# Kernel tuning notes

Hardware: AMD Instinct MI355X
Metric: run time of the kernel (lower is better)

Reference implementation:

```python
import jax, jax.numpy as jnp
import numpy as np

B, S, D, H = 2, 2048, 1024, 16
HD = D // H


def alibi_slopes(num_heads):
    x = (2.0 ** 8) ** (1.0 / num_heads)
    return jnp.array([1.0 / x ** (i + 1) for i in range(num_heads)], dtype=jnp.float32)


def setup_inputs() -> dict:
    key = jax.random.key(0)
    ks = jax.random.split(key, 5)
    scale = 1.0 / np.sqrt(D)
    return {
        "x": jax.random.normal(ks[0], (B, S, D), dtype=jnp.float32),
        "Wq": jax.random.normal(ks[1], (D, D), dtype=jnp.float32) * scale,
        "Wk": jax.random.normal(ks[2], (D, D), dtype=jnp.float32) * scale,
        "Wv": jax.random.normal(ks[3], (D, D), dtype=jnp.float32) * scale,
        "Wo": jax.random.normal(ks[4], (D, D), dtype=jnp.float32) * scale,
    }


def reference(x, Wq, Wk, Wv, Wo):
    b, s, d = x.shape
    # nn.Linear(bias=False): y = x @ W.T
    q = (x @ Wq.T).reshape(b, s, H, HD).transpose(0, 2, 1, 3)  # [b,h,s,hd]
    k = (x @ Wk.T).reshape(b, s, H, HD).transpose(0, 2, 1, 3)
    v = (x @ Wv.T).reshape(b, s, H, HD).transpose(0, 2, 1, 3)

    scores = jnp.einsum("bhqd,bhkd->bhqk", q, k) / jnp.sqrt(jnp.float32(HD))
    rel = (jnp.arange(s)[None, :] - jnp.arange(s)[:, None]).astype(jnp.float32)  # x - y
    m = alibi_slopes(H)[:, None, None]  # [h,1,1]
    scores = scores - (m * rel)[None]  # subtract bias, as in source

    causal_mask = jnp.tril(jnp.ones((s, s), dtype=bool))
    scores = jnp.where(causal_mask[None, None], scores, -jnp.inf)

    attn = jax.nn.softmax(scores, axis=-1)
    out = jnp.einsum("bhqk,bhkd->bhqd", attn, v)
    out = out.transpose(0, 2, 1, 3).reshape(b, s, d)
    return out @ Wo.T
```

## Files before the change

kernel.cpp:

```cpp
#include <hip/hip_runtime.h>

typedef __attribute__((ext_vector_type(8))) short bf16x8;
typedef __attribute__((ext_vector_type(4))) float f32x4;
typedef __attribute__((ext_vector_type(16))) float f32x16;
typedef __attribute__((ext_vector_type(8))) unsigned short u16x8;
typedef __attribute__((ext_vector_type(4))) unsigned short u16x4;
typedef __attribute__((ext_vector_type(2))) unsigned int uint2v;

#define MFMA_16x16x32(a, b, c) __builtin_amdgcn_mfma_f32_16x16x32_bf16((a), (b), (c), 0, 0, 0)
#define MFMA32(a, b, c) __builtin_amdgcn_mfma_f32_32x32x16_bf16((a), (b), (c), 0, 0, 0)

__device__ __forceinline__ unsigned short f2bf(float f) {
  unsigned u = __builtin_bit_cast(unsigned, f);
  u += 0x7fffu + ((u >> 16) & 1u);
  return (unsigned short)(u >> 16);
}

__device__ __forceinline__ void gload_lds16(const void* g, void* l) {
  __builtin_amdgcn_global_load_lds((__attribute__((address_space(1))) void*)(g),
                                   (__attribute__((address_space(3))) void*)(l),
                                   16, 0, 0);
}

__device__ __forceinline__ unsigned cvtpk(float lo, float hi) {
  unsigned r;
  asm("v_cvt_pk_bf16_f32 %0, %1, %2" : "=v"(r) : "v"(lo), "v"(hi));
  return r;
}

__global__ void cvt_bf16(const float* __restrict__ src, unsigned short* __restrict__ dst, int n4) {
  int i = blockIdx.x * blockDim.x + threadIdx.x;
  if (i >= n4) return;
  f32x4 v = *(const f32x4*)(src + (size_t)i * 4);
  u16x4 o;
  o.x = f2bf(v.x); o.y = f2bf(v.y); o.z = f2bf(v.z); o.w = f2bf(v.w);
  *(u16x4*)(dst + (size_t)i * 4) = o;
}

__global__ void cvt_w4(const float* __restrict__ s0, const float* __restrict__ s1,
                       const float* __restrict__ s2, const float* __restrict__ s3,
                       unsigned short* __restrict__ d0, unsigned short* __restrict__ d1,
                       unsigned short* __restrict__ d2, unsigned short* __restrict__ d3,
                       int n4) {
  const float* s; unsigned short* d;
  switch (blockIdx.y) {
    case 0: s = s0; d = d0; break;
    case 1: s = s1; d = d1; break;
    case 2: s = s2; d = d2; break;
    default: s = s3; d = d3; break;
  }
  int i = blockIdx.x * blockDim.x + threadIdx.x;
  if (i >= n4) return;
  f32x4 v = *(const f32x4*)(s + (size_t)i * 4);
  u16x4 o;
  o.x = f2bf(v.x); o.y = f2bf(v.y); o.z = f2bf(v.z); o.w = f2bf(v.w);
  *(u16x4*)(d + (size_t)i * 4) = o;
}

template <int OUTMODE>
__device__ __forceinline__ void gemm_body(const unsigned short* __restrict__ A,
                                          const unsigned short* __restrict__ Bw,
                                          void* __restrict__ Cout, float scale,
                                          int bx, int by) {
  constexpr int K = 1024, N = 1024;
  __shared__ unsigned short As[128 * 32];
  __shared__ unsigned short Bs[128 * 32];
  const int tid = threadIdx.x;
  const int lane = tid & 63;
  const int wave = tid >> 6;
  const int wm = (wave >> 1) * 64;
  const int wn = (wave & 1) * 64;
  const int l15 = lane & 15, lg = lane >> 4;

  f32x4 acc[4][4];
#pragma unroll
  for (int mi = 0; mi < 4; ++mi)
#pragma unroll
    for (int ni = 0; ni < 4; ++ni) acc[mi][ni] = (f32x4){0.f, 0.f, 0.f, 0.f};

  const int r0 = tid >> 2;
  const int c0 = (tid & 3) * 8;
  const unsigned short* Ag = A + (size_t)(by * 128 + r0) * K + c0;
  const unsigned short* Bg = Bw + (size_t)(bx * 128 + r0) * K + c0;
  unsigned short* lA = As + tid * 8;
  unsigned short* lB = Bs + tid * 8;

  for (int kt = 0; kt < K / 32; ++kt) {
    __syncthreads();
    gload_lds16(Ag + kt * 32, lA);
    gload_lds16(Ag + (size_t)64 * K + kt * 32, lA + 2048);
    gload_lds16(Bg + kt * 32, lB);
    gload_lds16(Bg + (size_t)64 * K + kt * 32, lB + 2048);
    __syncthreads();

    bf16x8 af[4], bf[4];
#pragma unroll
    for (int mi = 0; mi < 4; ++mi)
      af[mi] = *(const bf16x8*)&As[(wm + mi * 16 + l15) * 32 + lg * 8];
#pragma unroll
    for (int ni = 0; ni < 4; ++ni)
      bf[ni] = *(const bf16x8*)&Bs[(wn + ni * 16 + l15) * 32 + lg * 8];
#pragma unroll
    for (int mi = 0; mi < 4; ++mi)
#pragma unroll
      for (int ni = 0; ni < 4; ++ni)
        acc[mi][ni] = MFMA_16x16x32(af[mi], bf[ni], acc[mi][ni]);
  }

#pragma unroll
  for (int mi = 0; mi < 4; ++mi) {
    const int row = by * 128 + wm + mi * 16 + lg * 4;
#pragma unroll
    for (int ni = 0; ni < 4; ++ni) {
      const int col = bx * 128 + wn + ni * 16 + l15;
#pragma unroll
      for (int i = 0; i < 4; ++i) {
        float v = acc[mi][ni][i];
        if constexpr (OUTMODE == 0) {
          ((unsigned short*)Cout)[(size_t)(row + i) * N + col] = f2bf(v * scale);
        } else if constexpr (OUTMODE == 1) {
          const int m = row + i, n = col;
          ((unsigned short*)Cout)[(size_t)(((m >> 11) * 16 + (n >> 6)) * 64 + (n & 63)) * 2048 +
                                  (m & 2047)] = f2bf(v);
        } else {
          ((float*)Cout)[(size_t)(row + i) * N + col] = v;
        }
      }
    }
  }
}

__global__ __launch_bounds__(256) void gemm_qkv(const unsigned short* __restrict__ A,
                                                const unsigned short* __restrict__ Wq,
                                                const unsigned short* __restrict__ Wk,
                                                const unsigned short* __restrict__ Wv,
                                                unsigned short* __restrict__ Qo,
                                                unsigned short* __restrict__ Ko,
                                                unsigned short* __restrict__ Vo) {
  const int z = blockIdx.z;
  if (z == 0)      gemm_body<0>(A, Wq, Qo, 0.18033688011112042f, blockIdx.x, blockIdx.y);
  else if (z == 1) gemm_body<0>(A, Wk, Ko, 1.0f, blockIdx.x, blockIdx.y);
  else             gemm_body<1>(A, Wv, Vo, 1.0f, blockIdx.x, blockIdx.y);
}

__global__ __launch_bounds__(256) void gemm_out(const unsigned short* __restrict__ A,
                                                const unsigned short* __restrict__ Bw,
                                                float* __restrict__ C) {
  gemm_body<2>(A, Bw, C, 1.0f, blockIdx.x, blockIdx.y);
}

__global__ __launch_bounds__(256, 2) void attn_fwd(const unsigned short* __restrict__ Qg,
                                                   const unsigned short* __restrict__ Kg,
                                                   const unsigned short* __restrict__ Vtg,
                                                   unsigned short* __restrict__ Og) {
  constexpr int S = 2048;
  const int bid = blockIdx.x;
  const int xcd = bid & 7;
  const int ii = bid >> 3;
  const int hi2 = ii >> 5;
  const int jj = ii & 31;
  const int x = hi2 ? (15 - (jj & 15)) : (jj & 15);
  const int bh = xcd * 4 + hi2 * 2 + (jj >> 4);
  const int b = bh >> 4, h = bh & 15;

  const int lane = threadIdx.x & 63;
  const int wave = threadIdx.x >> 6;
  const int ql = lane & 31;
  const int H = lane >> 5;
  const int qw0 = x * 128 + wave * 32;
  const int qg = qw0 + ql;
  const float slope = exp2f(-0.5f * (float)(h + 1));
  const float sl2 = slope * 1.44269504088896f;

  bf16x8 qf[4];
  {
    const unsigned short* qp = Qg + (size_t)(b * S + qg) * 1024 + h * 64 + H * 8;
#pragma unroll
    for (int c = 0; c < 4; ++c) qf[c] = *(const bf16x8*)(qp + 16 * c);
  }

  f32x16 nbj;
#pragma unroll
  for (int r = 0; r < 16; ++r) {
    const float crow = (float)((r & 3) + 8 * (r >> 2) + 4 * H);
    nbj[r] = -sl2 * crow;
  }

  const unsigned short* kp0 = Kg + (size_t)(b * S + ql) * 1024 + h * 64 + H * 8;
  const unsigned short* kp1 = kp0 + (size_t)32 * 1024;
  const unsigned short* vp0 = Vtg + (size_t)(bh * 64 + ql) * S + H * 8;
  const unsigned short* vp1 = vp0 + (size_t)32 * S;

  f32x16 o0, o1;
#pragma unroll
  for (int r = 0; r < 16; ++r) { o0[r] = 0.f; o1[r] = 0.f; }
  float m = -1e30f, l = 0.f;

  const int nt = ((qw0 + 31) >> 6) + 1;
  for (int t = 0; t < nt; ++t) {
    const int k0 = t * 64;
    bf16x8 kf0[4], kf1[4], vf0[4], vf1[4];
#pragma unroll
    for (int c = 0; c < 4; ++c) {
      kf0[c] = *(const bf16x8*)(kp0 + 16 * c);
      kf1[c] = *(const bf16x8*)(kp1 + 16 * c);
      vf0[c] = *(const bf16x8*)(vp0 + 16 * c);
      vf1[c] = *(const bf16x8*)(vp1 + 16 * c);
    }
    kp0 += 65536; kp1 += 65536; vp0 += 64; vp1 += 64;

    f32x16 s0 = MFMA32(kf0[0], qf[0], nbj);
    f32x16 s1 = MFMA32(kf1[0], qf[0], nbj);
#pragma unroll
    for (int c = 1; c < 4; ++c) {
      s0 = MFMA32(kf0[c], qf[c], s0);
      s1 = MFMA32(kf1[c], qf[c], s1);
    }

    if (t == nt - 1) {
      const int qk = qg - k0 - 4 * H;
#pragma unroll
      for (int r = 0; r < 16; ++r) {
        const int crow = (r & 3) + 8 * (r >> 2);
        s0[r] = (crow > qk) ? -1e30f : s0[r];
        s1[r] = (crow + 32 > qk) ? -1e30f : s1[r];
      }
    }

    const float vb0 = sl2 * (float)k0;
    const float vb1 = sl2 * (float)(k0 + 32);
    float mx0 = s0[0], mx1 = s1[0];
#pragma unroll
    for (int r = 1; r < 16; ++r) { mx0 = fmaxf(mx0, s0[r]); mx1 = fmaxf(mx1, s1[r]); }
    float tmax = fmaxf(mx0 - vb0, mx1 - vb1);
    tmax = fmaxf(tmax, __shfl_xor(tmax, 32, 64));
    const float mnew = fmaxf(m, tmax);
    const float corr = __builtin_amdgcn_exp2f(m - mnew);
    m = mnew;
    const float e0 = vb0 + mnew, e1 = vb1 + mnew;

    f32x16 pp0, pp1;
#pragma unroll
    for (int r = 0; r < 16; ++r) {
      pp0[r] = __builtin_amdgcn_exp2f(s0[r] - e0);
      pp1[r] = __builtin_amdgcn_exp2f(s1[r] - e1);
    }
    float t8[8];
#pragma unroll
    for (int r = 0; r < 8; ++r) t8[r] = (pp0[r] + pp0[r + 8]) + (pp1[r] + pp1[r + 8]);
    float tsum = ((t8[0] + t8[1]) + (t8[2] + t8[3])) + ((t8[4] + t8[5]) + (t8[6] + t8[7]));
    tsum += __shfl_xor(tsum, 32, 64);
    l = l * corr + tsum;

#pragma unroll
    for (int r = 0; r < 16; ++r) { o0[r] *= corr; o1[r] *= corr; }

#pragma unroll
    for (int ck = 0; ck < 4; ++ck) {
      const int c = ck & 1;
      unsigned w0, w1, w2, w3;
      if (ck < 2) {
        w0 = cvtpk(pp0[8 * c + 0], pp0[8 * c + 1]);
        w1 = cvtpk(pp0[8 * c + 2], pp0[8 * c + 3]);
        w2 = cvtpk(pp0[8 * c + 4], pp0[8 * c + 5]);
        w3 = cvtpk(pp0[8 * c + 6], pp0[8 * c + 7]);
      } else {
        w0 = cvtpk(pp1[8 * c + 0], pp1[8 * c + 1]);
        w1 = cvtpk(pp1[8 * c + 2], pp1[8 * c + 3]);
        w2 = cvtpk(pp1[8 * c + 4], pp1[8 * c + 5]);
        w3 = cvtpk(pp1[8 * c + 6], pp1[8 * c + 7]);
      }
      unsigned sa = H ? w0 : w2;
      unsigned sb = H ? w1 : w3;
      sa = (unsigned)__shfl_xor((int)sa, 32, 64);
      sb = (unsigned)__shfl_xor((int)sb, 32, 64);
      union { unsigned u[4]; bf16x8 v; } fr;
      fr.u[0] = H ? sa : w0;
      fr.u[1] = H ? sb : w1;
      fr.u[2] = H ? w2 : sa;
      fr.u[3] = H ? w3 : sb;
      o0 = MFMA32(vf0[ck], fr.v, o0);
      o1 = MFMA32(vf1[ck], fr.v, o1);
    }
  }

  const float rl = __builtin_amdgcn_rcpf(l);
  unsigned short* ob = Og + (size_t)(b * S + qg) * 1024 + h * 64 + 4 * H;
#pragma unroll
  for (int a2 = 0; a2 < 4; ++a2) {
    uint2v w01, w23;
    w01.x = cvtpk(o0[4 * a2 + 0] * rl, o0[4 * a2 + 1] * rl);
    w01.y = cvtpk(o0[4 * a2 + 2] * rl, o0[4 * a2 + 3] * rl);
    w23.x = cvtpk(o1[4 * a2 + 0] * rl, o1[4 * a2 + 1] * rl);
    w23.y = cvtpk(o1[4 * a2 + 2] * rl, o1[4 * a2 + 3] * rl);
    *(uint2v*)(ob + 8 * a2) = w01;
    *(uint2v*)(ob + 32 + 8 * a2) = w23;
  }
}

extern "C" void kernel_launch(void* const* d_in, const int* in_sizes, int n_in,
                              void* d_out, int out_size, void* d_ws, size_t ws_size,
                              hipStream_t stream) {
  const float* x = (const float*)d_in[0];
  const float* Wq = (const float*)d_in[1];
  const float* Wk = (const float*)d_in[2];
  const float* Wv = (const float*)d_in[3];
  const float* Wo = (const float*)d_in[4];

  unsigned short* xb = (unsigned short*)d_ws;
  unsigned short* Wqb = xb + 4194304;
  unsigned short* Wkb = Wqb + 1048576;
  unsigned short* Wvb = Wkb + 1048576;
  unsigned short* Wob = Wvb + 1048576;
  unsigned short* Qb = Wob + 1048576;
  unsigned short* Kb = Qb + 4194304;
  unsigned short* Vtb = Kb + 4194304;
  unsigned short* Ob = Vtb + 4194304;

  cvt_bf16<<<4096, 256, 0, stream>>>(x, xb, 1048576);
  cvt_w4<<<dim3(1024, 4), 256, 0, stream>>>(Wq, Wk, Wv, Wo, Wqb, Wkb, Wvb, Wob, 262144);

  gemm_qkv<<<dim3(8, 32, 3), 256, 0, stream>>>(xb, Wqb, Wkb, Wvb, Qb, Kb, Vtb);

  attn_fwd<<<512, 256, 0, stream>>>(Qb, Kb, Vtb, Ob);

  gemm_out<<<dim3(8, 32), 256, 0, stream>>>(Ob, Wob, (float*)d_out);
}
```

Before: 212.0 us.

## Split attention KV range across waves with LDS combine and double-buffered loads

Each block now handles one 32-row query tile, and its four waves split the causal KV range into chunks, each running its own online softmax. The per-wave max, sum and output partials are merged through shared memory, with serialized accumulation across the waves. K/V fragment loads are double-buffered across tiles, and s_setprio is raised around the MFMAs. The goal is more parallelism (2048 blocks instead of 512) and better latency hiding. The cost is more redundant Q loads, LDS traffic and barriers, and higher register pressure.

```diff
diff --git a/kernel.cpp b/kernel.cpp
--- a/kernel.cpp
+++ b/kernel.cpp
@@ -149,26 +149,116 @@
   gemm_body<2>(A, Bw, C, 1.0f, blockIdx.x, blockIdx.y);
 }
 
+
+#define LOADT(KA, KB, VA, VB, tt)                                          \
+  {                                                                        \
+    const unsigned short* _kp = kbase + (size_t)(tt) * 65536;              \
+    const unsigned short* _vp = vbase + (size_t)(tt) * 64;                 \
+    _Pragma("unroll")                                                      \
+    for (int c = 0; c < 4; ++c) {                                          \
+      KA[c] = *(const bf16x8*)(_kp + 16 * c);                              \
+      KB[c] = *(const bf16x8*)(_kp + 32768 + 16 * c);                      \
+      VA[c] = *(const bf16x8*)(_vp + 16 * c);                              \
+      VB[c] = *(const bf16x8*)(_vp + 65536 + 16 * c);                      \
+    }                                                                      \
+  }
+
+#define COMPT(KA, KB, VA, VB, tt, MASKED)                                      \
+  {                                                                            \
+    const int _k0 = (tt) * 64;                                                 \
+    __builtin_amdgcn_s_setprio(1);                                             \
+    f32x16 _s0 = MFMA32(KA[0], qf[0], nbj);                                    \
+    f32x16 _s1 = MFMA32(KB[0], qf[0], nbj);                                    \
+    _s0 = MFMA32(KA[1], qf[1], _s0); _s1 = MFMA32(KB[1], qf[1], _s1);          \
+    _s0 = MFMA32(KA[2], qf[2], _s0); _s1 = MFMA32(KB[2], qf[2], _s1);          \
+    _s0 = MFMA32(KA[3], qf[3], _s0); _s1 = MFMA32(KB[3], qf[3], _s1);          \
+    __builtin_amdgcn_s_setprio(0);                                             \
+    if (MASKED) {                                                              \
+      const int _qk = qg - _k0 - 4 * H;                                        \
+      _Pragma("unroll")                                                        \
+      for (int r = 0; r < 16; ++r) {                                           \
+        const int _cr = (r & 3) + 8 * (r >> 2);                                \
+        _s0[r] = (_cr > _qk) ? -1e30f : _s0[r];                                \
+        _s1[r] = (_cr + 32 > _qk) ? -1e30f : _s1[r];                           \
+      }                                                                        \
+    }                                                                          \
+    const float _vb0 = sl2 * (float)_k0;                                       \
+    const float _vb1 = sl2 * (float)(_k0 + 32);                                \
+    float _mx0 = _s0[0], _mx1 = _s1[0];                                        \
+    _Pragma("unroll")                                                          \
+    for (int r = 1; r < 16; ++r) { _mx0 = fmaxf(_mx0, _s0[r]); _mx1 = fmaxf(_mx1, _s1[r]); } \
+    float _tmax = fmaxf(_mx0 - _vb0, _mx1 - _vb1);                             \
+    _tmax = fmaxf(_tmax, __shfl_xor(_tmax, 32, 64));                           \
+    const float _mnew = fmaxf(m, _tmax);                                       \
+    const float _corr = __builtin_amdgcn_exp2f(m - _mnew);                     \
+    m = _mnew;                                                                 \
+    const float _e0 = _vb0 + _mnew, _e1 = _vb1 + _mnew;                        \
+    f32x16 _pp0, _pp1;                                                         \
+    _Pragma("unroll")                                                          \
+    for (int r = 0; r < 16; ++r) {                                             \
+      _pp0[r] = __builtin_amdgcn_exp2f(_s0[r] - _e0);                          \
+      _pp1[r] = __builtin_amdgcn_exp2f(_s1[r] - _e1);                          \
+    }                                                                          \
+    float _t8[8];                                                              \
+    _Pragma("unroll")                                                          \
+    for (int r = 0; r < 8; ++r) _t8[r] = (_pp0[r] + _pp0[r + 8]) + (_pp1[r] + _pp1[r + 8]); \
+    float _tsum = ((_t8[0] + _t8[1]) + (_t8[2] + _t8[3])) + ((_t8[4] + _t8[5]) + (_t8[6] + _t8[7])); \
+    _tsum += __shfl_xor(_tsum, 32, 64);                                        \
+    l = l * _corr + _tsum;                                                     \
+    _Pragma("unroll")                                                          \
+    for (int r = 0; r < 16; ++r) { o0[r] *= _corr; o1[r] *= _corr; }           \
+    _Pragma("unroll")                                                          \
+    for (int ck = 0; ck < 4; ++ck) {                                           \
+      const int _c = ck & 1;                                                   \
+      unsigned _w0, _w1, _w2, _w3;                                             \
+      if (ck < 2) {                                                            \
+        _w0 = cvtpk(_pp0[8 * _c + 0], _pp0[8 * _c + 1]);                       \
+        _w1 = cvtpk(_pp0[8 * _c + 2], _pp0[8 * _c + 3]);                       \
+        _w2 = cvtpk(_pp0[8 * _c + 4], _pp0[8 * _c + 5]);                       \
+        _w3 = cvtpk(_pp0[8 * _c + 6], _pp0[8 * _c + 7]);                       \
+      } else {                                                                 \
+        _w0 = cvtpk(_pp1[8 * _c + 0], _pp1[8 * _c + 1]);                       \
+        _w1 = cvtpk(_pp1[8 * _c + 2], _pp1[8 * _c + 3]);                       \
+        _w2 = cvtpk(_pp1[8 * _c + 4], _pp1[8 * _c + 5]);                       \
+        _w3 = cvtpk(_pp1[8 * _c + 6], _pp1[8 * _c + 7]);                       \
+      }                                                                        \
+      unsigned _sa = H ? _w0 : _w2;                                            \
+      unsigned _sb = H ? _w1 : _w3;                                            \
+      _sa = (unsigned)__shfl_xor((int)_sa, 32, 64);                            \
+      _sb = (unsigned)__shfl_xor((int)_sb, 32, 64);                            \
+      union { unsigned u[4]; bf16x8 v; } _fr;                                  \
+      _fr.u[0] = H ? _sa : _w0;                                                \
+      _fr.u[1] = H ? _sb : _w1;                                                \
+      _fr.u[2] = H ? _w2 : _sa;                                                \
+      _fr.u[3] = H ? _w3 : _sb;                                                \
+      __builtin_amdgcn_s_setprio(1);                                           \
+      o0 = MFMA32(VA[ck], _fr.v, o0);                                          \
+      o1 = MFMA32(VB[ck], _fr.v, o1);                                          \
+      __builtin_amdgcn_s_setprio(0);                                           \
+    }                                                                          \
+  }
+
 __global__ __launch_bounds__(256, 2) void attn_fwd(const unsigned short* __restrict__ Qg,
                                                    const unsigned short* __restrict__ Kg,
                                                    const unsigned short* __restrict__ Vtg,
                                                    unsigned short* __restrict__ Og) {
   constexpr int S = 2048;
+  __shared__ float Ml[4][64];
+  __shared__ float Ll[4][64];
+  __shared__ float Oacc[64][33];
+
   const int bid = blockIdx.x;
   const int xcd = bid & 7;
-  const int ii = bid >> 3;
-  const int hi2 = ii >> 5;
-  const int jj = ii & 31;
-  const int x = hi2 ? (15 - (jj & 15)) : (jj & 15);
-  const int bh = xcd * 4 + hi2 * 2 + (jj >> 4);
+  const int ord = bid >> 3;
+  const int qt = 63 - (ord >> 2);
+  const int bh = xcd * 4 + (ord & 3);
   const int b = bh >> 4, h = bh & 15;
 
   const int lane = threadIdx.x & 63;
   const int wave = threadIdx.x >> 6;
   const int ql = lane & 31;
   const int H = lane >> 5;
-  const int qw0 = x * 128 + wave * 32;
-  const int qg = qw0 + ql;
+  const int qg = qt * 32 + ql;
   const float slope = exp2f(-0.5f * (float)(h + 1));
   const float sl2 = slope * 1.44269504088896f;
 
@@ -186,115 +276,84 @@
     nbj[r] = -sl2 * crow;
   }
 
-  const unsigned short* kp0 = Kg + (size_t)(b * S + ql) * 1024 + h * 64 + H * 8;
-  const unsigned short* kp1 = kp0 + (size_t)32 * 1024;
-  const unsigned short* vp0 = Vtg + (size_t)(bh * 64 + ql) * S + H * 8;
-  const unsigned short* vp1 = vp0 + (size_t)32 * S;
+  const unsigned short* kbase = Kg + (size_t)(b * S + ql) * 1024 + h * 64 + H * 8;
+  const unsigned short* vbase = Vtg + (size_t)(bh * 64 + ql) * S + H * 8;
 
   f32x16 o0, o1;
 #pragma unroll
   for (int r = 0; r < 16; ++r) { o0[r] = 0.f; o1[r] = 0.f; }
   float m = -1e30f, l = 0.f;
 
-  const int nt = ((qw0 + 31) >> 6) + 1;
-  for (int t = 0; t < nt; ++t) {
-    const int k0 = t * 64;
-    bf16x8 kf0[4], kf1[4], vf0[4], vf1[4];
-#pragma unroll
-    for (int c = 0; c < 4; ++c) {
-      kf0[c] = *(const bf16x8*)(kp0 + 16 * c);
-      kf1[c] = *(const bf16x8*)(kp1 + 16 * c);
-      vf0[c] = *(const bf16x8*)(vp0 + 16 * c);
-      vf1[c] = *(const bf16x8*)(vp1 + 16 * c);
-    }
-    kp0 += 65536; kp1 += 65536; vp0 += 64; vp1 += 64;
-
-    f32x16 s0 = MFMA32(kf0[0], qf[0], nbj);
-    f32x16 s1 = MFMA32(kf1[0], qf[0], nbj);
-#pragma unroll
-    for (int c = 1; c < 4; ++c) {
-      s0 = MFMA32(kf0[c], qf[c], s0);
-      s1 = MFMA32(kf1[c], qf[c], s1);
-    }
-
-    if (t == nt - 1) {
-      const int qk = qg - k0 - 4 * H;
-#pragma unroll
-      for (int r = 0; r < 16; ++r) {
-        const int crow = (r & 3) + 8 * (r >> 2);
-        s0[r] = (crow > qk) ? -1e30f : s0[r];
-        s1[r] = (crow + 32 > qk) ? -1e30f : s1[r];
+  const int nt = (qt >> 1) + 1;
+  const int cs = (nt + 3) >> 2;
+  const int t0 = wave * cs;
+  const int te = min(nt, t0 + cs);
+
+  bf16x8 ka0[4], ka1[4], vA0[4], vA1[4];
+  bf16x8 kb0[4], kb1[4], vB0[4], vB1[4];
+
+  if (t0 < te) {
+    LOADT(ka0, ka1, vA0, vA1, t0);
+    int t = t0;
+    for (; t + 1 < te; ++t) {
+      if ((t - t0) & 1) {
+        LOADT(ka0, ka1, vA0, vA1, t + 1);
+        COMPT(kb0, kb1, vB0, vB1, t, false);
+      } else {
+        LOADT(kb0, kb1, vB0, vB1, t + 1);
+        COMPT(ka0, ka1, vA0, vA1, t, false);
       }
     }
-
-    const float vb0 = sl2 * (float)k0;
-    const float vb1 = sl2 * (float)(k0 + 32);
-    float mx0 = s0[0], mx1 = s1[0];
-#pragma unroll
-    for (int r = 1; r < 16; ++r) { mx0 = fmaxf(mx0, s0[r]); mx1 = fmaxf(mx1, s1[r]); }
-    float tmax = fmaxf(mx0 - vb0, mx1 - vb1);
-    tmax = fmaxf(tmax, __shfl_xor(tmax, 32, 64));
-    const float mnew = fmaxf(m, tmax);
-    const float corr = __builtin_amdgcn_exp2f(m - mnew);
-    m = mnew;
-    const float e0 = vb0 + mnew, e1 = vb1 + mnew;
-
-    f32x16 pp0, pp1;
-#pragma unroll
-    for (int r = 0; r < 16; ++r) {
-      pp0[r] = __builtin_amdgcn_exp2f(s0[r] - e0);
-      pp1[r] = __builtin_amdgcn_exp2f(s1[r] - e1);
+    const bool msk = (te == nt);
+    if ((t - t0) & 1) {
+      COMPT(kb0, kb1, vB0, vB1, t, msk);
+    } else {
+      COMPT(ka0, ka1, vA0, vA1, t, msk);
     }
-    float t8[8];
-#pragma unroll
-    for (int r = 0; r < 8; ++r) t8[r] = (pp0[r] + pp0[r + 8]) + (pp1[r] + pp1[r + 8]);
-    float tsum = ((t8[0] + t8[1]) + (t8[2] + t8[3])) + ((t8[4] + t8[5]) + (t8[6] + t8[7]));
-    tsum += __shfl_xor(tsum, 32, 64);
-    l = l * corr + tsum;
-
-#pragma unroll
-    for (int r = 0; r < 16; ++r) { o0[r] *= corr; o1[r] *= corr; }
-
-#pragma unroll
-    for (int ck = 0; ck < 4; ++ck) {
-      const int c = ck & 1;
-      unsigned w0, w1, w2, w3;
-      if (ck < 2) {
-        w0 = cvtpk(pp0[8 * c + 0], pp0[8 * c + 1]);
-        w1 = cvtpk(pp0[8 * c + 2], pp0[8 * c + 3]);
-        w2 = cvtpk(pp0[8 * c + 4], pp0[8 * c + 5]);
-        w3 = cvtpk(pp0[8 * c + 6], pp0[8 * c + 7]);
-      } else {
-        w0 = cvtpk(pp1[8 * c + 0], pp1[8 * c + 1]);
-        w1 = cvtpk(pp1[8 * c + 2], pp1[8 * c + 3]);
-        w2 = cvtpk(pp1[8 * c + 4], pp1[8 * c + 5]);
-        w3 = cvtpk(pp1[8 * c + 6], pp1[8 * c + 7]);
-      }
-      unsigned sa = H ? w0 : w2;
-      unsigned sb = H ? w1 : w3;
-      sa = (unsigned)__shfl_xor((int)sa, 32, 64);
-      sb = (unsigned)__shfl_xor((int)sb, 32, 64);
-      union { unsigned u[4]; bf16x8 v; } fr;
-      fr.u[0] = H ? sa : w0;
-      fr.u[1] = H ? sb : w1;
-      fr.u[2] = H ? w2 : sa;
-      fr.u[3] = H ? w3 : sb;
-      o0 = MFMA32(vf0[ck], fr.v, o0);
-      o1 = MFMA32(vf1[ck], fr.v, o1);
+  }
+
+  Ml[wave][lane] = m;
+  Ll[wave][lane] = l;
+  __syncthreads();
+  const float M = fmaxf(fmaxf(Ml[0][lane], Ml[1][lane]), fmaxf(Ml[2][lane], Ml[3][lane]));
+  const float ci = __builtin_amdgcn_exp2f(m - M);
+  float lt = Ll[0][lane] * __builtin_amdgcn_exp2f(Ml[0][lane] - M);
+  lt += Ll[1][lane] * __builtin_amdgcn_exp2f(Ml[1][lane] - M);
+  lt += Ll[2][lane] * __builtin_amdgcn_exp2f(Ml[2][lane] - M);
+  lt += Ll[3][lane] * __builtin_amdgcn_exp2f(Ml[3][lane] - M);
+#pragma unroll
+  for (int r = 0; r < 16; ++r) { o0[r] *= ci; o1[r] *= ci; }
+
+  if (wave == 0) {
+#pragma unroll
+    for (int r = 0; r < 16; ++r) { Oacc[lane][r] = o0[r]; Oacc[lane][16 + r] = o1[r]; }
+  }
+  __syncthreads();
+  if (wave == 1) {
+#pragma unroll
+    for (int r = 0; r < 16; ++r) { Oacc[lane][r] += o0[r]; Oacc[lane][16 + r] += o1[r]; }
+  }
+  __syncthreads();
+  if (wave == 2) {
+#pragma unroll
+    for (int r = 0; r < 16; ++r) { Oacc[lane][r] += o0[r]; Oacc[lane][16 + r] += o1[r]; }
+  }
+  __syncthreads();
+  if (wave == 3) {
+#pragma unroll
+    for (int r = 0; r < 16; ++r) { o0[r] += Oacc[lane][r]; o1[r] += Oacc[lane][16 + r]; }
+    const float rl = 1.0f / lt;
+    unsigned short* ob = Og + (size_t)(b * S + qg) * 1024 + h * 64 + 4 * H;
+#pragma unroll
+    for (int a2 = 0; a2 < 4; ++a2) {
+      uint2v w01, w23;
+      w01.x = cvtpk(o0[4 * a2 + 0] * rl, o0[4 * a2 + 1] * rl);
+      w01.y = cvtpk(o0[4 * a2 + 2] * rl, o0[4 * a2 + 3] * rl);
+      w23.x = cvtpk(o1[4 * a2 + 0] * rl, o1[4 * a2 + 1] * rl);
+      w23.y = cvtpk(o1[4 * a2 + 2] * rl, o1[4 * a2 + 3] * rl);
+      *(uint2v*)(ob + 8 * a2) = w01;
+      *(uint2v*)(ob + 32 + 8 * a2) = w23;
     }
-  }
-
-  const float rl = __builtin_amdgcn_rcpf(l);
-  unsigned short* ob = Og + (size_t)(b * S + qg) * 1024 + h * 64 + 4 * H;
-#pragma unroll
-  for (int a2 = 0; a2 < 4; ++a2) {
-    uint2v w01, w23;
-    w01.x = cvtpk(o0[4 * a2 + 0] * rl, o0[4 * a2 + 1] * rl);
-    w01.y = cvtpk(o0[4 * a2 + 2] * rl, o0[4 * a2 + 3] * rl);
-    w23.x = cvtpk(o1[4 * a2 + 0] * rl, o1[4 * a2 + 1] * rl);
-    w23.y = cvtpk(o1[4 * a2 + 2] * rl, o1[4 * a2 + 3] * rl);
-    *(uint2v*)(ob + 8 * a2) = w01;
-    *(uint2v*)(ob + 32 + 8 * a2) = w23;
   }
 }
 
@@ -322,7 +381,7 @@
 
   gemm_qkv<<<dim3(8, 32, 3), 256, 0, stream>>>(xb, Wqb, Wkb, Wvb, Qb, Kb, Vtb);
 
-  attn_fwd<<<512, 256, 0, stream>>>(Qb, Kb, Vtb, Ob);
+  attn_fwd<<<2048, 256, 0, stream>>>(Qb, Kb, Vtb, Ob);
 
   gemm_out<<<dim3(8, 32), 256, 0, stream>>>(Ob, Wob, (float*)d_out);
 }
```

Measured after the change: 367.8 us. 73.5% more time.
